# Performance work log

Measured on AMD Instinct MI355X. Metric: run time of the kernel, lower is better.

Reference implementation:

```python
import jax, jax.numpy as jnp
import numpy as np


def setup_inputs() -> dict:
    key = jax.random.key(0)
    kx, ky = jax.random.split(key)
    B, C, T = 4, 2, 32768
    x = jax.random.normal(kx, (B, C, T), dtype=jnp.float32)
    y = jax.random.normal(ky, (B, C, T), dtype=jnp.float32)
    return {"x": x, "y": y, "max_shift": 128}


def reference(x, y, max_shift):
    # x: (B, C, T), y: (B, C, T) (or any suffix shape broadcastable from the right)
    T = x.shape[-1]
    S = 2 * max_shift + 1  # number of shift windows
    # pad last dim by max_shift on each side
    pad_cfg = [(0, 0)] * (x.ndim - 1) + [(max_shift, max_shift)]
    x_pad = jnp.pad(x, pad_cfg)
    # unfold into S overlapping windows of length T, stride 1
    idx = jnp.arange(S)[:, None] + jnp.arange(T)[None, :]  # (S, T)
    xw = x_pad[..., idx]                 # (B, C, S, T)
    xw = jnp.moveaxis(xw, -2, 0)         # (S, B, C, T)
    # center each window and y along time
    xw = xw - xw.mean(-1, keepdims=True)
    yc = y - y.mean(-1, keepdims=True)
    corr = (xw * yc).sum(-1)                               # (S, B, C)
    norm = (xw ** 2).sum(-1) * (yc ** 2).sum(-1)           # (S, B, C)
    return corr / jnp.sqrt(norm)
```

## Files before the change

### kernel.cpp

```cpp
#include <hip/hip_runtime.h>
#include <math.h>

#define MAX_SHIFT 128
#define S_TOTAL   257
#define SGB       8
#define NSB       33
#define TY        4096
#define VY        8
#define XT        (TY + 16)

__global__ __launch_bounds__(256) void spc_kernel(const float* __restrict__ x,
                                                  const float* __restrict__ y,
                                                  float* __restrict__ out,
                                                  int T, int BC) {
    const int sg  = blockIdx.x;
    const int bc  = blockIdx.y;
    const int s0  = sg * SGB;
    const int d0  = s0 - MAX_SHIFT;
    const int tid = threadIdx.x;
    const float* xb = x + (size_t)bc * T;
    const float* yb = y + (size_t)bc * T;
    const int NCH = T / TY;

    __shared__ __align__(16) float xs[XT];
    __shared__ float red[SGB + 4][4];
    __shared__ float edge[SGB][2];

    float acc[SGB];
#pragma unroll
    for (int j = 0; j < SGB; ++j) acc[j] = 0.f;
    float sx = 0.f, sxx = 0.f, sy = 0.f, syy = 0.f;

    for (int c = 0; c < NCH; ++c) {
        const int t0 = c * TY;
        const int G0 = t0 + d0;

        __syncthreads();
        for (int ls = tid * 4; ls < XT; ls += 1024) {
            int g = G0 + ls;
            float4 v;
            if (g >= 0 && g + 3 < T) {
                v = *(const float4*)(xb + g);
            } else {
                float tmp[4];
#pragma unroll
                for (int e = 0; e < 4; ++e) {
                    int gg = g + e;
                    tmp[e] = (gg >= 0 && gg < T) ? xb[gg] : 0.f;
                }
                v = make_float4(tmp[0], tmp[1], tmp[2], tmp[3]);
            }
            *(float4*)(xs + ls) = v;
        }
        __syncthreads();

#pragma unroll
        for (int k = 0; k < TY / (256 * VY); ++k) {
            const int b = k * (256 * VY) + tid * VY;
            const int t = t0 + b;
            float yv[VY], xv[VY], xw[VY + SGB];
            *(float4*)(yv)     = *(const float4*)(yb + t);
            *(float4*)(yv + 4) = *(const float4*)(yb + t + 4);
            *(float4*)(xv)     = *(const float4*)(xb + t);
            *(float4*)(xv + 4) = *(const float4*)(xb + t + 4);
#pragma unroll
            for (int i = 0; i < (VY + SGB) / 4; ++i)
                *(float4*)(xw + 4 * i) = *(const float4*)(xs + b + 4 * i);

#pragma unroll
            for (int e = 0; e < VY; ++e) {
#pragma unroll
                for (int j = 0; j < SGB; ++j)
                    acc[j] = fmaf(xw[e + j], yv[e], acc[j]);
                sy += yv[e]; syy = fmaf(yv[e], yv[e], syy);
                sx += xv[e]; sxx = fmaf(xv[e], xv[e], sxx);
            }
        }
    }

    const int lane = tid & 63, wave = tid >> 6;
#pragma unroll
    for (int j = 0; j < SGB; ++j) {
        float v = acc[j];
        for (int off = 32; off; off >>= 1) v += __shfl_down(v, off, 64);
        if (lane == 0) red[j][wave] = v;
    }
    {
        float v4[4] = {sx, sxx, sy, syy};
#pragma unroll
        for (int q = 0; q < 4; ++q) {
            float v = v4[q];
            for (int off = 32; off; off >>= 1) v += __shfl_down(v, off, 64);
            if (lane == 0) red[SGB + q][wave] = v;
        }
    }

    for (int sl = wave; sl < SGB; sl += 4) {
        int d = d0 + sl;
        float pw = 0.f, pw2 = 0.f;
        if (d > 0) {
            for (int j = lane; j < d; j += 64) { float v = xb[j];         pw += v; pw2 = fmaf(v, v, pw2); }
        } else if (d < 0) {
            for (int j = lane; j < -d; j += 64) { float v = xb[T + d + j]; pw += v; pw2 = fmaf(v, v, pw2); }
        }
        for (int off = 32; off; off >>= 1) {
            pw  += __shfl_down(pw,  off, 64);
            pw2 += __shfl_down(pw2, off, 64);
        }
        if (lane == 0) { edge[sl][0] = pw; edge[sl][1] = pw2; }
    }
    __syncthreads();

    if (tid < SGB) {
        int s = s0 + tid;
        if (s < S_TOTAL) {
            float cr  = red[tid][0] + red[tid][1] + red[tid][2] + red[tid][3];
            float Sx  = red[SGB + 0][0] + red[SGB + 0][1] + red[SGB + 0][2] + red[SGB + 0][3];
            float Sxx = red[SGB + 1][0] + red[SGB + 1][1] + red[SGB + 1][2] + red[SGB + 1][3];
            float Sy  = red[SGB + 2][0] + red[SGB + 2][1] + red[SGB + 2][2] + red[SGB + 2][3];
            float Syy = red[SGB + 3][0] + red[SGB + 3][1] + red[SGB + 3][2] + red[SGB + 3][3];
            float Sw  = Sx  - edge[tid][0];
            float Sw2 = Sxx - edge[tid][1];
            float invT  = 1.0f / (float)T;
            float corr  = cr  - Sw * Sy * invT;
            float normx = Sw2 - Sw * Sw * invT;
            float normy = Syy - Sy * Sy * invT;
            out[(size_t)s * BC + bc] = corr / sqrtf(normx * normy);
        }
    }
}

extern "C" void kernel_launch(void* const* d_in, const int* in_sizes, int n_in,
                              void* d_out, int out_size, void* d_ws, size_t ws_size,
                              hipStream_t stream) {
    const float* x = (const float*)d_in[0];
    const float* y = (const float*)d_in[1];
    float* out = (float*)d_out;

    const int BC = out_size / S_TOTAL;
    const int T  = in_sizes[0] / BC;

    dim3 grid(NSB, BC);
    spc_kernel<<<grid, 256, 0, stream>>>(x, y, out, T, BC);
}
```

Measured before the change: 80.26 us.

## Use 1024-thread blocks with 9 shifts per block and aligned shared tile

```diff
diff --git a/kernel.cpp b/kernel.cpp
--- a/kernel.cpp
+++ b/kernel.cpp
@@ -3,27 +3,32 @@
 
 #define MAX_SHIFT 128
 #define S_TOTAL   257
-#define SGB       8
-#define NSB       33
-#define TY        4096
+#define SGB       9
+#define NSB       29
+#define BLOCK     1024
+#define TY        8192
 #define VY        8
-#define XT        (TY + 16)
+#define XT        8208
+#define NQ        (SGB + 4)
 
-__global__ __launch_bounds__(256) void spc_kernel(const float* __restrict__ x,
-                                                  const float* __restrict__ y,
-                                                  float* __restrict__ out,
-                                                  int T, int BC) {
-    const int sg  = blockIdx.x;
-    const int bc  = blockIdx.y;
-    const int s0  = sg * SGB;
-    const int d0  = s0 - MAX_SHIFT;
-    const int tid = threadIdx.x;
+__global__ __launch_bounds__(BLOCK) void spc_kernel(const float* __restrict__ x,
+                                                    const float* __restrict__ y,
+                                                    float* __restrict__ out,
+                                                    int T, int BC) {
+    const int sg    = blockIdx.x;
+    const int bc    = blockIdx.y;
+    const int s0    = sg * SGB;
+    const int d0    = s0 - MAX_SHIFT;
+    const int d0r   = d0 & ~3;
+    const int delta = d0 - d0r;
+    const int tid   = threadIdx.x;
     const float* xb = x + (size_t)bc * T;
     const float* yb = y + (size_t)bc * T;
     const int NCH = T / TY;
 
     __shared__ __align__(16) float xs[XT];
-    __shared__ float red[SGB + 4][4];
+    __shared__ float red[NQ][16];
+    __shared__ float tot[NQ];
     __shared__ float edge[SGB][2];
 
     float acc[SGB];
@@ -33,10 +38,10 @@
 
     for (int c = 0; c < NCH; ++c) {
         const int t0 = c * TY;
-        const int G0 = t0 + d0;
+        const int G0 = t0 + d0r;
 
         __syncthreads();
-        for (int ls = tid * 4; ls < XT; ls += 1024) {
+        for (int ls = tid * 4; ls < XT; ls += BLOCK * 4) {
             int g = G0 + ls;
             float4 v;
             if (g >= 0 && g + 3 < T) {
@@ -54,25 +59,25 @@
         }
         __syncthreads();
 
-#pragma unroll
-        for (int k = 0; k < TY / (256 * VY); ++k) {
-            const int b = k * (256 * VY) + tid * VY;
+        {
+            const int b = tid * VY;
             const int t = t0 + b;
-            float yv[VY], xv[VY], xw[VY + SGB];
+            float yv[VY], xv[VY], xw[20];
             *(float4*)(yv)     = *(const float4*)(yb + t);
             *(float4*)(yv + 4) = *(const float4*)(yb + t + 4);
             *(float4*)(xv)     = *(const float4*)(xb + t);
             *(float4*)(xv + 4) = *(const float4*)(xb + t + 4);
 #pragma unroll
-            for (int i = 0; i < (VY + SGB) / 4; ++i)
+            for (int i = 0; i < 5; ++i)
                 *(float4*)(xw + 4 * i) = *(const float4*)(xs + b + 4 * i);
 
 #pragma unroll
             for (int e = 0; e < VY; ++e) {
+                const float yvv = yv[e];
 #pragma unroll
                 for (int j = 0; j < SGB; ++j)
-                    acc[j] = fmaf(xw[e + j], yv[e], acc[j]);
-                sy += yv[e]; syy = fmaf(yv[e], yv[e], syy);
+                    acc[j] = fmaf(xw[delta + e + j], yvv, acc[j]);
+                sy += yvv; syy = fmaf(yvv, yvv, syy);
                 sx += xv[e]; sxx = fmaf(xv[e], xv[e], sxx);
             }
         }
@@ -95,11 +100,12 @@
         }
     }
 
-    for (int sl = wave; sl < SGB; sl += 4) {
+    if (wave < SGB) {
+        const int sl = wave;
         int d = d0 + sl;
         float pw = 0.f, pw2 = 0.f;
         if (d > 0) {
-            for (int j = lane; j < d; j += 64) { float v = xb[j];         pw += v; pw2 = fmaf(v, v, pw2); }
+            for (int j = lane; j < d; j += 64)  { float v = xb[j];         pw += v; pw2 = fmaf(v, v, pw2); }
         } else if (d < 0) {
             for (int j = lane; j < -d; j += 64) { float v = xb[T + d + j]; pw += v; pw2 = fmaf(v, v, pw2); }
         }
@@ -111,14 +117,22 @@
     }
     __syncthreads();
 
+    if (tid < NQ) {
+        float v = 0.f;
+#pragma unroll
+        for (int w = 0; w < 16; ++w) v += red[tid][w];
+        tot[tid] = v;
+    }
+    __syncthreads();
+
     if (tid < SGB) {
         int s = s0 + tid;
         if (s < S_TOTAL) {
-            float cr  = red[tid][0] + red[tid][1] + red[tid][2] + red[tid][3];
-            float Sx  = red[SGB + 0][0] + red[SGB + 0][1] + red[SGB + 0][2] + red[SGB + 0][3];
-            float Sxx = red[SGB + 1][0] + red[SGB + 1][1] + red[SGB + 1][2] + red[SGB + 1][3];
-            float Sy  = red[SGB + 2][0] + red[SGB + 2][1] + red[SGB + 2][2] + red[SGB + 2][3];
-            float Syy = red[SGB + 3][0] + red[SGB + 3][1] + red[SGB + 3][2] + red[SGB + 3][3];
+            float cr  = tot[tid];
+            float Sx  = tot[SGB + 0];
+            float Sxx = tot[SGB + 1];
+            float Sy  = tot[SGB + 2];
+            float Syy = tot[SGB + 3];
             float Sw  = Sx  - edge[tid][0];
             float Sw2 = Sxx - edge[tid][1];
             float invT  = 1.0f / (float)T;
@@ -141,5 +155,5 @@
     const int T  = in_sizes[0] / BC;
 
     dim3 grid(NSB, BC);
-    spc_kernel<<<grid, 256, 0, stream>>>(x, y, out, T, BC);
+    spc_kernel<<<grid, BLOCK, 0, stream>>>(x, y, out, T, BC);
 }
```

After: 87.89 us. 1.1x slower.
